# Optimization experiments

Measured on AMD Instinct MI355X. Metric: run time of the kernel, lower is better.

## Reference

```python
import jax, jax.numpy as jnp
import numpy as np

WS = 8      # window size
SS = 4      # shift size
NH = 4      # num heads
EPS = 1e-5
MLP_RATIO = 4


def _win_part(x, ws):
    # x: [B,D,H,W,C] -> [B*nD*nH*nW, ws^3, C]
    B, D, H, W, C = x.shape
    x = x.reshape(B, D // ws, ws, H // ws, ws, W // ws, ws, C)
    x = x.transpose(0, 1, 3, 5, 2, 4, 6, 7)
    return x.reshape(-1, ws * ws * ws, C)


def _win_rev(w, ws, B, D, H, W):
    C = w.shape[-1]
    x = w.reshape(B, D // ws, H // ws, W // ws, ws, ws, ws, C)
    x = x.transpose(0, 1, 4, 2, 5, 3, 6, 7)
    return x.reshape(B, D, H, W, C)


def _ln(x, g, b):
    m = jnp.mean(x, axis=-1, keepdims=True)
    v = jnp.mean((x - m) ** 2, axis=-1, keepdims=True)
    return (x - m) / jnp.sqrt(v + EPS) * g + b


def _rel_index(ws):
    coords = np.stack(np.meshgrid(np.arange(ws), np.arange(ws), np.arange(ws), indexing='ij'))  # [3,ws,ws,ws]
    cf = coords.reshape(3, -1)                      # [3, ws^3]
    rel = (cf[:, :, None] - cf[:, None, :]).transpose(1, 2, 0) + (ws - 1)  # [N,N,3]
    return rel[..., 0] * (2 * ws - 1) ** 2 + rel[..., 1] * (2 * ws - 1) + rel[..., 2]


def _attn_mask(D, H, W, ws, ss):
    img = np.zeros((1, D, H, W, 1), dtype=np.float32)
    cnt = 0
    sl = (slice(0, -ws), slice(-ws, -ss), slice(-ss, None))
    for d in sl:
        for h in sl:
            for w in sl:
                img[:, d, h, w, :] = cnt
                cnt += 1
    mw = np.asarray(_win_part(jnp.asarray(img), ws))[..., 0]  # [nW, ws^3]
    diff = mw[:, None, :] - mw[:, :, None]
    return np.where(diff != 0, -100.0, 0.0).astype(np.float32)


def setup_inputs() -> dict:
    key = jax.random.key(0)
    ks = jax.random.split(key, 12)
    B, D, H, W, C = 1, 16, 64, 64, 128
    mh = MLP_RATIO * C
    s = 0.02
    return {
        'x': jax.random.normal(ks[0], (B, D, H, W, C), jnp.float32),
        'attn_mask': jnp.asarray(_attn_mask(D, H, W, WS, SS)),
        'rel_index': jnp.asarray(_rel_index(WS), jnp.int32),
        'rel_bias': jax.random.normal(ks[1], ((2 * WS - 1) ** 3, NH), jnp.float32) * s,
        'qkv_w': jax.random.normal(ks[2], (3 * C, C), jnp.float32) * s,
        'qkv_b': jnp.zeros((3 * C,), jnp.float32),
        'proj_w': jax.random.normal(ks[3], (C, C), jnp.float32) * s,
        'proj_b': jnp.zeros((C,), jnp.float32),
        'norm1_g': jnp.ones((C,), jnp.float32),
        'norm1_b': jnp.zeros((C,), jnp.float32),
        'norm2_g': jnp.ones((C,), jnp.float32),
        'norm2_b': jnp.zeros((C,), jnp.float32),
        'mlp_w1': jax.random.normal(ks[4], (mh, C), jnp.float32) * s,
        'mlp_b1': jnp.zeros((mh,), jnp.float32),
        'mlp_w2': jax.random.normal(ks[5], (C, mh), jnp.float32) * s,
        'mlp_b2': jnp.zeros((C,), jnp.float32),
    }


def reference(x, attn_mask, rel_index, rel_bias, qkv_w, qkv_b, proj_w, proj_b,
              norm1_g, norm1_b, norm2_g, norm2_b, mlp_w1, mlp_b1, mlp_w2, mlp_b2):
    B, D, H, W, C = x.shape
    ws, ss, nh = WS, SS, NH
    hd = C // nh
    scale = hd ** -0.5
    N = ws ** 3
    shortcut = x
    h = _ln(x, norm1_g, norm1_b)
    h = jnp.roll(h, (-ss, -ss, -ss), axis=(1, 2, 3))
    xw = _win_part(h, ws)                 # [B_, N, C]
    B_ = xw.shape[0]
    nW = attn_mask.shape[0]
    qkv = xw @ qkv_w.T + qkv_b            # [B_, N, 3C]
    qkv = qkv.reshape(B_, N, 3, nh, hd).transpose(2, 0, 3, 1, 4)  # [3,B_,h,N,hd]
    q, k, v = qkv[0] * scale, qkv[1], qkv[2]
    attn = jnp.einsum('bhnd,bhmd->bhnm', q, k)
    rpe = rel_bias[rel_index.reshape(-1)].reshape(N, N, nh).transpose(2, 0, 1)  # [h,N,N]
    attn = attn + rpe[None]
    attn = attn.reshape(B_ // nW, nW, nh, N, N) + attn_mask[None, :, None]
    attn = jax.nn.softmax(attn.reshape(B_, nh, N, N), axis=-1)
    out = jnp.einsum('bhnm,bhmd->bhnd', attn, v).transpose(0, 2, 1, 3).reshape(B_, N, C)
    out = out @ proj_w.T + proj_b
    out = _win_rev(out, ws, B, D, H, W)
    out = jnp.roll(out, (ss, ss, ss), axis=(1, 2, 3))
    x = shortcut + out
    h2 = _ln(x, norm2_g, norm2_b)
    h2 = jax.nn.gelu(h2 @ mlp_w1.T + mlp_b1, approximate=False)
    return x + h2 @ mlp_w2.T + mlp_b2
```

## Files before the change

### kernel.cpp

```cpp
#include <hip/hip_runtime.h>
#include <math.h>

typedef __bf16 bf16;
typedef __bf16 bf16x4 __attribute__((ext_vector_type(4)));
typedef __bf16 bf16x8 __attribute__((ext_vector_type(8)));
typedef float f32x4 __attribute__((ext_vector_type(4)));
typedef unsigned short u16;
typedef u16 u16x2 __attribute__((ext_vector_type(2)));

#define LOG2E 1.4426950408889634f

__device__ __forceinline__ float b2f(u16 b) {
  return (float)__builtin_bit_cast(bf16, b);
}

__global__ void sniff_k(const unsigned* __restrict__ xw_, int* __restrict__ flag) {
  int lane = threadIdx.x;
  int c = 0;
#pragma unroll
  for (int j = 0; j < 4; j++) {
    unsigned e = (xw_[lane * 4 + j] >> 7) & 0xFFu;
    c += (e >= 100u && e <= 140u) ? 1 : 0;
  }
#pragma unroll
  for (int d = 1; d < 64; d <<= 1) c += __shfl_xor(c, d);
  if (lane == 0) *flag = (c >= 150) ? 1 : 0;
}

__global__ __launch_bounds__(256) void canon_norm_k(
    const void* __restrict__ sg, const void* __restrict__ sb,
    bf16* __restrict__ dg, bf16* __restrict__ db, const int* __restrict__ flag) {
  int i = threadIdx.x;
  int fl = *flag;
  if (i < 128) {
    dg[i] = fl ? ((const bf16*)sg)[i] : (bf16)((const float*)sg)[i];
  } else {
    int j = i - 128;
    db[j] = fl ? ((const bf16*)sb)[j] : (bf16)((const float*)sb)[j];
  }
}

struct ProArgs {
  const int* ridx;
  const void* rbias;
  bf16* rpem;
  const void* x;
  const bf16* g1;
  const bf16* b1n;
  bf16* xw;
  const void* csrc[12];
  bf16* cdst[12];
  int cn[12];
};

__global__ __launch_bounds__(256) void pro_k(ProArgs a,
                                             const int* __restrict__ flag) {
  const int bx = blockIdx.x, tid = threadIdx.x;
  const int fl = *flag;
  if (bx < 8192) {
    int t = bx * 256 + tid;
    int m0 = (t & 127) * 4, q = (t >> 7) & 511, h = (t >> 16) & 3, ty = t >> 18;
    int qd = q >> 6, qh = (q >> 3) & 7, qw = q & 7;
    int kt = m0 >> 6, mt = (m0 >> 4) & 3, quad = (m0 >> 2) & 3;
    int4 ri = *(const int4*)&a.ridx[q * 512 + m0];
    const int rv[4] = {ri.x, ri.y, ri.z, ri.w};
    bf16x4 o;
#pragma unroll
    for (int j = 0; j < 4; j++) {
      int m = m0 + j;
      int md = m >> 6, mh = (m >> 3) & 7, mw = m & 7;
      bool diff = ((ty & 4) && ((qd < 4) != (md < 4))) ||
                  ((ty & 2) && ((qh < 4) != (mh < 4))) ||
                  ((ty & 1) && ((qw < 4) != (mw < 4)));
      float bv = fl ? (float)((const bf16*)a.rbias)[rv[j] * 4 + h]
                    : ((const float*)a.rbias)[rv[j] * 4 + h];
      float v = bv * LOG2E;
      o[j] = (bf16)(v + (diff ? -144.2695041f : 0.f));
    }
    size_t out = ((size_t)(ty * 4 + h) << 18) +
                 (((size_t)(kt * 4 + quad) * 512 + q) * 16 + mt * 4);
    *(bf16x4*)&a.rpem[out] = o;
  } else if (bx < 24576) {
    int wave = tid >> 6, lane = tid & 63;
    int tok = (bx - 8192) * 4 + wave;
    int win = tok >> 9, pos = tok & 511;
    int rd = (win >> 6) * 8 + (pos >> 6);
    int rh = ((win >> 3) & 7) * 8 + ((pos >> 3) & 7);
    int rw = (win & 7) * 8 + (pos & 7);
    int od = (rd + 4) & 15, oh = (rh + 4) & 63, ow = (rw + 4) & 63;
    size_t src = (size_t)((od * 64 + oh) * 64 + ow) * 128;
    int ch = lane * 2;
    float f0, f1;
    if (!fl) {
      const float* xf = (const float*)a.x + src + ch;
      f0 = xf[0];
      f1 = xf[1];
    } else {
      u16x2 xv = *(const u16x2*)((const bf16*)a.x + src + ch);
      f0 = b2f(xv[0]);
      f1 = b2f(xv[1]);
    }
    float s = f0 + f1, sq = f0 * f0 + f1 * f1;
#pragma unroll
    for (int d = 1; d < 64; d <<= 1) {
      s += __shfl_xor(s, d);
      sq += __shfl_xor(sq, d);
    }
    float mean = s * (1.f / 128.f);
    float var = sq * (1.f / 128.f) - mean * mean;
    float rstd = rsqrtf(fmaxf(var, 0.f) + 1e-5f);
    u16x2 gv = *(const u16x2*)(a.g1 + ch), bv = *(const u16x2*)(a.b1n + ch);
    u16x2 ov;
    ov[0] =
        __builtin_bit_cast(u16, (bf16)((f0 - mean) * rstd * b2f(gv[0]) + b2f(bv[0])));
    ov[1] =
        __builtin_bit_cast(u16, (bf16)((f1 - mean) * rstd * b2f(gv[1]) + b2f(bv[1])));
    *(u16x2*)(a.xw + (size_t)tok * 128 + ch) = ov;
  } else {
    int seg = bx - 24576;
    int ti = seg >> 8;
    int i = (seg & 255) * 256 + tid;
    if (i < a.cn[ti]) {
      if (fl)
        a.cdst[ti][i] = ((const bf16*)a.csrc[ti])[i];
      else
        a.cdst[ti][i] = (bf16)((const float*)a.csrc[ti])[i];
    }
  }
}

template <int EPI, int BM, int BK, int N_, int K_>
__global__ __launch_bounds__(256) void gemm_k(const bf16* __restrict__ A,
                                              const bf16* __restrict__ B,
                                              const bf16* __restrict__ bias,
                                              void* __restrict__ outv,
                                              const void* __restrict__ residv,
                                              const int* __restrict__ flag) {
  constexpr int NC = K_ / BK;
  constexpr int NBUF = (NC > 1) ? 2 : 1;
  __shared__ __align__(16) u16 SM[NBUF][(BM + 128) * BK];
  const int t = threadIdx.x;
  const int wave = t >> 6, lane = t & 63, l15 = lane & 15, quad = lane >> 4;
  const int m0 = blockIdx.x * BM, n0 = blockIdx.y * 128;
  constexpr int MI = BM / 32;
  int fl = 0;
  if constexpr (EPI == 1) fl = *flag;
  f32x4 acc[MI][4] = {};
  const int wr = (wave >> 1) * (BM / 2), wc = (wave & 1) * 64;
  constexpr int TPR = BK / 8;
  constexpr int RPP = 256 / TPR;
  constexpr int PASSES = (BM + 128) / RPP;
  const int srow = t / TPR, sc16 = t % TPR;

  auto stage = [&](int c, int buf) {
#pragma unroll
    for (int p = 0; p < PASSES; p++) {
      int row = p * RPP + srow;
      int cs = sc16 ^ (row & 7);
      const u16* src;
      if (row < BM)
        src = (const u16*)A + (size_t)(m0 + row) * K_ + c * BK + cs * 8;
      else
        src = (const u16*)B + (size_t)(n0 + row - BM) * K_ + c * BK + cs * 8;
      __builtin_amdgcn_global_load_lds(
          (const __attribute__((address_space(1))) void*)src,
          (__attribute__((address_space(3))) void*)&SM[buf][row * BK + sc16 * 8],
          16, 0, 0);
    }
  };

  stage(0, 0);
  __syncthreads();
#pragma unroll
  for (int c = 0; c < NC; c++) {
    if (c + 1 < NC) stage(c + 1, (c + 1) & 1);
    const char* cur = (const char*)SM[c & 1];
#pragma unroll
    for (int ks = 0; ks < BK / 32; ks++) {
      bf16x8 a[MI], b[4];
#pragma unroll
      for (int i = 0; i < MI; i++) {
        int row = wr + i * 16 + l15;
        a[i] = *(const bf16x8*)(cur + row * (BK * 2) +
                                (((ks * 4 + quad) ^ (row & 7)) << 4));
      }
#pragma unroll
      for (int j = 0; j < 4; j++) {
        int row = BM + wc + j * 16 + l15;
        b[j] = *(const bf16x8*)(cur + row * (BK * 2) +
                                (((ks * 4 + quad) ^ (row & 7)) << 4));
      }
#pragma unroll
      for (int i = 0; i < MI; i++)
#pragma unroll
        for (int j = 0; j < 4; j++)
          acc[i][j] =
              __builtin_amdgcn_mfma_f32_16x16x32_bf16(a[i], b[j], acc[i][j], 0, 0, 0);
    }
    if (c + 1 < NC) __syncthreads();
  }
  const float qscale = 0.17677669529663687f * LOG2E;
#pragma unroll
  for (int i = 0; i < MI; i++) {
#pragma unroll
    for (int r = 0; r < 4; r++) {
      int tok = m0 + wr + i * 16 + quad * 4 + r;
      size_t obase = 0;
      if constexpr (EPI == 1) {
        int win = tok >> 9, pos = tok & 511;
        int rd = (win >> 6) * 8 + (pos >> 6);
        int rh = ((win >> 3) & 7) * 8 + ((pos >> 3) & 7);
        int rw = (win & 7) * 8 + (pos & 7);
        int od = (rd + 4) & 15, oh = (rh + 4) & 63, ow = (rw + 4) & 63;
        obase = (size_t)((od * 64 + oh) * 64 + ow) * 128;
      }
#pragma unroll
      for (int j = 0; j < 4; j++) {
        int gn = n0 + wc + j * 16 + l15;
        float v = acc[i][j][r] + (float)bias[gn];
        if constexpr (EPI == 0) {
          int tensor = gn >> 7, c = gn & 127, head = c >> 5, d = c & 31;
          if (tensor == 0) v *= qscale;
          int win = tok >> 9, pos = tok & 511;
          size_t off = ((((size_t)tensor * 4 + head) * 128 + win) * 512 + pos) * 32 + d;
          ((bf16*)outv)[off] = (bf16)v;
        } else {
          float rs = fl ? (float)((const bf16*)residv)[obase + gn]
                        : ((const float*)residv)[obase + gn];
          v += rs;
          ((bf16*)outv)[obase + gn] = (bf16)v;
        }
      }
    }
  }
}

__global__ __launch_bounds__(256) void mlp_k(const bf16* __restrict__ X2,
                                             const bf16* __restrict__ G2,
                                             const bf16* __restrict__ B2n,
                                             const bf16* __restrict__ W1,
                                             const bf16* __restrict__ B1,
                                             const bf16* __restrict__ W2,
                                             const bf16* __restrict__ B2,
                                             void* __restrict__ outv,
                                             const int* __restrict__ flag) {
  __shared__ __align__(16) u16 sA[32 * 128];
  __shared__ __align__(16) u16 sB[128 * 128];
  __shared__ __align__(16) u16 sH[32 * 520];
  const int t = threadIdx.x;
  const int wave = t >> 6, lane = t & 63, l15 = lane & 15, quad = lane >> 4;
  const int m0 = blockIdx.x * 32;
  const int wr = (wave >> 1) * 16, wc = (wave & 1) * 64;
  const int fl = *flag;
  const int srow = t >> 4, sc16 = t & 15;

  {
#pragma unroll
    for (int p = 0; p < 2; p++) {
      int row = p * 16 + srow;
      int cs = sc16 ^ (row & 7);
      __builtin_amdgcn_global_load_lds(
          (const __attribute__((address_space(1))) void*)((const u16*)X2 +
                                                          (size_t)(m0 + row) * 128 +
                                                          cs * 8),
          (__attribute__((address_space(3))) void*)&sA[row * 128 + sc16 * 8], 16,
          0, 0);
    }
#pragma unroll
    for (int p = 0; p < 8; p++) {
      int row = p * 16 + srow;
      int cs = sc16 ^ (row & 7);
      __builtin_amdgcn_global_load_lds(
          (const __attribute__((address_space(1))) void*)((const u16*)W1 +
                                                          (size_t)row * 128 +
                                                          cs * 8),
          (__attribute__((address_space(3))) void*)&sB[row * 128 + sc16 * 8], 16,
          0, 0);
    }
  }
  __syncthreads();

  {
    int r = t >> 3, k = t & 7;
    bf16x8 c0 = *(const bf16x8*)&sA[r * 128 + (k * 2 + 0) * 8];
    bf16x8 c1 = *(const bf16x8*)&sA[r * 128 + (k * 2 + 1) * 8];
    float s = 0.f, sq = 0.f;
#pragma unroll
    for (int e = 0; e < 8; e++) {
      float f0 = (float)c0[e], f1 = (float)c1[e];
      s += f0 + f1;
      sq += f0 * f0 + f1 * f1;
    }
#pragma unroll
    for (int d = 1; d < 8; d <<= 1) {
      s += __shfl_xor(s, d);
      sq += __shfl_xor(sq, d);
    }
    float mean = s * (1.f / 128.f);
    float var = sq * (1.f / 128.f) - mean * mean;
    float rstd = rsqrtf(fmaxf(var, 0.f) + 1e-5f);
    __syncthreads();
#pragma unroll
    for (int j = 0; j < 2; j++) {
      int tc = ((k * 2 + j) ^ (r & 7)) * 8;
      bf16x8 gv = *(const bf16x8*)&G2[tc];
      bf16x8 bv = *(const bf16x8*)&B2n[tc];
      bf16x8 cv = j ? c1 : c0;
      bf16x8 ov;
#pragma unroll
      for (int e = 0; e < 8; e++)
        ov[e] = (bf16)(((float)cv[e] - mean) * rstd * (float)gv[e] + (float)bv[e]);
      *(bf16x8*)&sA[r * 128 + (k * 2 + j) * 8] = ov;
    }
  }
  __syncthreads();

  bf16x8 wreg[8];

#pragma unroll 1
  for (int nc = 0; nc < 4; nc++) {
    {
      const bf16* Wn = (nc < 3) ? W1 : W2;
      const int chunk = (nc < 3) ? nc + 1 : 0;
      const int wK = (nc < 3) ? 128 : 512;
#pragma unroll
      for (int p = 0; p < 8; p++) {
        int row = p * 16 + srow;
        int cs = sc16 ^ (row & 7);
        const u16* src = (const u16*)Wn +
                         (size_t)(wK == 128 ? (chunk * 128 + row) : row) * wK +
                         (wK == 128 ? 0 : chunk * 128) + cs * 8;
        wreg[p] = *(const bf16x8*)src;
      }
    }
    f32x4 acc1[4] = {};
#pragma unroll
    for (int ks = 0; ks < 4; ks++) {
      int arow = wr + l15;
      bf16x8 av = *(const bf16x8*)((const char*)sA + arow * 256 +
                                   (((ks * 4 + quad) ^ (arow & 7)) << 4));
      bf16x8 bv[4];
#pragma unroll
      for (int j = 0; j < 4; j++) {
        int row = wc + j * 16 + l15;
        bv[j] = *(const bf16x8*)((const char*)sB + row * 256 +
                                 (((ks * 4 + quad) ^ (row & 7)) << 4));
      }
#pragma unroll
      for (int j = 0; j < 4; j++)
        acc1[j] = __builtin_amdgcn_mfma_f32_16x16x32_bf16(av, bv[j], acc1[j], 0, 0, 0);
    }
#pragma unroll
    for (int j = 0; j < 4; j++) {
      int ncol = nc * 128 + wc + j * 16 + l15;
      float bj = (float)B1[ncol];
#pragma unroll
      for (int r = 0; r < 4; r++) {
        float v = acc1[j][r] + bj;
        float v2 = v * v;
        float u2 = v * (2.30220806f + 0.10294323f * v2);
        float e2 = exp2f(u2);
        v = v - v * __builtin_amdgcn_rcpf(e2 + 1.f);
        sH[(wr + quad * 4 + r) * 520 + ncol] = __builtin_bit_cast(u16, (bf16)v);
      }
    }
    __syncthreads();
#pragma unroll
    for (int p = 0; p < 8; p++) {
      int row = p * 16 + srow;
      *(bf16x8*)&sB[row * 128 + sc16 * 8] = wreg[p];
    }
    __syncthreads();
  }

  f32x4 acc2[4] = {};
#pragma unroll 1
  for (int kc = 0; kc < 4; kc++) {
    if (kc < 3) {
      const int chunk = kc + 1;
#pragma unroll
      for (int p = 0; p < 8; p++) {
        int row = p * 16 + srow;
        int cs = sc16 ^ (row & 7);
        const u16* src =
            (const u16*)W2 + (size_t)row * 512 + chunk * 128 + cs * 8;
        wreg[p] = *(const bf16x8*)src;
      }
    }
#pragma unroll
    for (int ks = 0; ks < 4; ks++) {
      int arow = wr + l15;
      bf16x8 av = *(const bf16x8*)((const char*)sH + arow * 1040 +
                                   (kc * 128 + ks * 32 + quad * 8) * 2);
#pragma unroll
      for (int j = 0; j < 4; j++) {
        int row = wc + j * 16 + l15;
        bf16x8 bv = *(const bf16x8*)((const char*)sB + row * 256 +
                                     (((ks * 4 + quad) ^ (row & 7)) << 4));
        acc2[j] = __builtin_amdgcn_mfma_f32_16x16x32_bf16(av, bv, acc2[j], 0, 0, 0);
      }
    }
    if (kc < 3) {
      __syncthreads();
#pragma unroll
      for (int p = 0; p < 8; p++) {
        int row = p * 16 + srow;
        *(bf16x8*)&sB[row * 128 + sc16 * 8] = wreg[p];
      }
      __syncthreads();
    }
  }
#pragma unroll
  for (int j = 0; j < 4; j++) {
    int gn = wc + j * 16 + l15;
    float bj = (float)B2[gn];
#pragma unroll
    for (int r = 0; r < 4; r++) {
      int tok = m0 + wr + quad * 4 + r;
      size_t off = (size_t)tok * 128 + gn;
      float v = acc2[j][r] + bj + (float)X2[off];
      if (fl)
        ((bf16*)outv)[off] = (bf16)v;
      else
        ((float*)outv)[off] = v;
    }
  }
}

__global__ __launch_bounds__(512, 4) void attn_k(const bf16* __restrict__ qkv,
                                                 const bf16* __restrict__ rpem,
                                                 bf16* __restrict__ att) {
  __shared__ __align__(16) bf16 sVt[32 * 512];
  __shared__ __align__(16) bf16 sP[8][32 * 64];
  const int t = threadIdx.x;
  const int p = blockIdx.x;
  const int win = ((p >> 5) << 3) | (p & 7);
  const int head = (p >> 3) & 3;
  const int wave = t >> 6, lane = t & 63, l15 = lane & 15, quad = lane >> 4;

  const int wd = win >> 6, wh = (win >> 3) & 7, ww = win & 7;
  const int type = ((wd == 1) << 2) | ((wh == 7) << 1) | (ww == 7);

  const size_t hw32 = (size_t)512 * 32;
  const bf16* qp = qkv + ((size_t)(0 * 4 + head) * 128 + win) * hw32;
  const bf16* kp = qkv + ((size_t)(1 * 4 + head) * 128 + win) * hw32;
  const bf16* vp = qkv + ((size_t)(2 * 4 + head) * 128 + win) * hw32;
  const bf16* rpeh = rpem + ((size_t)(type * 4 + head) << 18);

  {
    int kpi = t >> 3, dblk = (t & 7) * 4;
    char* sb = (char*)sVt;
#pragma unroll
    for (int kb = 0; kb < 4; kb++) {
      const bf16* v0 = vp + (size_t)(kb * 128 + 2 * kpi) * 32 + dblk;
      bf16x4 a = *(const bf16x4*)v0;
      bf16x4 b = *(const bf16x4*)(v0 + 32);
      int keyw = kb * 64 + kpi;
#pragma unroll
      for (int dd = 0; dd < 4; dd++) {
        int row = dblk + dd;
        unsigned wv = (unsigned)__builtin_bit_cast(u16, a[dd]) |
                      ((unsigned)__builtin_bit_cast(u16, b[dd]) << 16);
        *(unsigned*)(sb + ((row * 1024 + keyw * 4) ^ ((row & 7) << 4))) = wv;
      }
    }
  }

  bf16x8 ones;
#pragma unroll
  for (int e = 0; e < 8; e++) ones[e] = (bf16)1.0f;

  __syncthreads();

  char* pw = (char*)sP[wave];
  const char* sv = (const char*)sVt;
  const int swz = (l15 & 7) << 4;

#pragma unroll 1
  for (int qh = 0; qh < 2; qh++) {
    const int qbase = qh * 256 + wave * 32;
    bf16x8 qa[2];
#pragma unroll
    for (int nt = 0; nt < 2; nt++)
      qa[nt] =
          *(const bf16x8*)(qp + (size_t)(qbase + nt * 16 + l15) * 32 + quad * 8);

    f32x4 O[2][2] = {};
    f32x4 O2[2] = {};

#pragma unroll 1
    for (int kt = 0; kt < 8; kt++) {
      bf16x8 kb[4];
      bf16x8 rv8[2][2];
#pragma unroll
      for (int mt = 0; mt < 4; mt++)
        kb[mt] = *(const bf16x8*)(kp + (size_t)(kt * 64 + mt * 16 + l15) * 32 +
                                  quad * 8);
#pragma unroll
      for (int nt = 0; nt < 2; nt++) {
        const bf16* rb =
            rpeh + ((size_t)(kt * 4 + quad) * 512 + (qbase + nt * 16 + l15)) * 16;
        rv8[nt][0] = *(const bf16x8*)rb;
        rv8[nt][1] = *(const bf16x8*)(rb + 8);
      }
      f32x4 S[4][2];
#pragma unroll
      for (int mt = 0; mt < 4; mt++)
#pragma unroll
        for (int nt = 0; nt < 2; nt++) {
          f32x4 c;
#pragma unroll
          for (int r = 0; r < 4; r++)
            c[r] = (float)rv8[nt][mt >> 1][(mt & 1) * 4 + r];
          S[mt][nt] =
              __builtin_amdgcn_mfma_f32_16x16x32_bf16(kb[mt], qa[nt], c, 0, 0, 0);
        }
#pragma unroll
      for (int nt = 0; nt < 2; nt++)
#pragma unroll
        for (int mt = 0; mt < 4; mt++) {
          bf16x4 pv;
#pragma unroll
          for (int r = 0; r < 4; r++) pv[r] = (bf16)exp2f(S[mt][nt][r]);
          *(bf16x4*)(pw + (((nt * 16 + l15) * 128 + mt * 32 + quad * 8) ^ swz)) =
              pv;
        }
#pragma unroll
      for (int s = 0; s < 2; s++) {
        int vc = kt * 128 + s * 64 + quad * 16;
        int pc = s * 64 + quad * 16;
        bf16x8 va0 = *(const bf16x8*)(sv + ((l15 * 1024 + vc) ^ swz));
        bf16x8 va1 = *(const bf16x8*)(sv + (((16 + l15) * 1024 + vc) ^ swz));
        bf16x8 pb0 = *(const bf16x8*)(pw + ((l15 * 128 + pc) ^ swz));
        bf16x8 pb1 = *(const bf16x8*)(pw + (((16 + l15) * 128 + pc) ^ swz));
        O[0][0] = __builtin_amdgcn_mfma_f32_16x16x32_bf16(va0, pb0, O[0][0], 0, 0, 0);
        O[0][1] = __builtin_amdgcn_mfma_f32_16x16x32_bf16(va0, pb1, O[0][1], 0, 0, 0);
        O[1][0] = __builtin_amdgcn_mfma_f32_16x16x32_bf16(va1, pb0, O[1][0], 0, 0, 0);
        O[1][1] = __builtin_amdgcn_mfma_f32_16x16x32_bf16(va1, pb1, O[1][1], 0, 0, 0);
        O2[0] = __builtin_amdgcn_mfma_f32_16x16x32_bf16(ones, pb0, O2[0], 0, 0, 0);
        O2[1] = __builtin_amdgcn_mfma_f32_16x16x32_bf16(ones, pb1, O2[1], 0, 0, 0);
      }
    }
#pragma unroll
    for (int nt = 0; nt < 2; nt++) {
      float inv = __builtin_amdgcn_rcpf(O2[nt][0]);
      int q = qbase + nt * 16 + l15;
#pragma unroll
      for (int dm = 0; dm < 2; dm++) {
        bf16x4 o;
#pragma unroll
        for (int r = 0; r < 4; r++) o[r] = (bf16)(O[dm][nt][r] * inv);
        *(bf16x4*)(att + ((size_t)win * 512 + q) * 128 + head * 32 + dm * 16 +
                   quad * 4) = o;
      }
    }
  }
}

extern "C" void kernel_launch(void* const* d_in, const int* in_sizes, int n_in,
                              void* d_out, int out_size, void* d_ws,
                              size_t ws_size, hipStream_t stream) {
  const int* rel_index = (const int*)d_in[2];
  char* w = (char*)d_ws;

  int* flag = (int*)w;
  bf16* qw_c = (bf16*)(w + (128ull << 10));
  bf16* pw_c = (bf16*)(w + (256ull << 10));
  bf16* w1_c = (bf16*)(w + (320ull << 10));
  bf16* w2_c = (bf16*)(w + (512ull << 10));
  bf16* qb_c = (bf16*)(w + (704ull << 10));
  bf16* pb_c = (bf16*)(w + (708ull << 10));
  bf16* g1_c = (bf16*)(w + (712ull << 10));
  bf16* b1n_c = (bf16*)(w + (716ull << 10));
  bf16* g2_c = (bf16*)(w + (720ull << 10));
  bf16* b2n_c = (bf16*)(w + (724ull << 10));
  bf16* mb1_c = (bf16*)(w + (728ull << 10));
  bf16* mb2_c = (bf16*)(w + (732ull << 10));
  bf16* xw = (bf16*)(w + (17ull << 20));
  bf16* qkvb = (bf16*)(w + (33ull << 20));
  bf16* x2 = (bf16*)(w + (99ull << 20));
  bf16* rpem = x2;
  bf16* att = xw;

  sniff_k<<<1, 64, 0, stream>>>((const unsigned*)d_in[0], flag);
  canon_norm_k<<<1, 256, 0, stream>>>(d_in[8], d_in[9], g1_c, b1n_c, flag);

  ProArgs pa;
  pa.ridx = rel_index;
  pa.rbias = d_in[3];
  pa.rpem = rpem;
  pa.x = d_in[0];
  pa.g1 = g1_c;
  pa.b1n = b1n_c;
  pa.xw = xw;
  const int srcidx[12] = {4, 5, 6, 7, 8, 9, 10, 11, 12, 13, 14, 15};
  bf16* dsts[12] = {qw_c, qb_c, pw_c, pb_c, g1_c, b1n_c,
                    g2_c, b2n_c, w1_c, mb1_c, w2_c, mb2_c};
  for (int i = 0; i < 12; i++) {
    pa.csrc[i] = d_in[srcidx[i]];
    pa.cdst[i] = dsts[i];
    pa.cn[i] = in_sizes[srcidx[i]];
  }
  pro_k<<<27648, 256, 0, stream>>>(pa, flag);

  gemm_k<0, 32, 128, 384, 128><<<dim3(2048, 3), 256, 0, stream>>>(
      xw, qw_c, qb_c, qkvb, nullptr, flag);
  attn_k<<<512, 512, 0, stream>>>(qkvb, rpem, att);
  gemm_k<1, 32, 128, 128, 128><<<dim3(2048, 1), 256, 0, stream>>>(
      att, pw_c, pb_c, x2, d_in[0], flag);
  mlp_k<<<2048, 256, 0, stream>>>(x2, g2_c, b2n_c, w1_c, mb1_c, w2_c, mb2_c,
                                  d_out, flag);
}
```

Before: 376.3 us.

## Fuse LayerNorm1, shift and window gather into the QKV GEMM prologue

```diff
diff --git a/kernel.cpp b/kernel.cpp
--- a/kernel.cpp
+++ b/kernel.cpp
@@ -27,27 +27,10 @@
   if (lane == 0) *flag = (c >= 150) ? 1 : 0;
 }
 
-__global__ __launch_bounds__(256) void canon_norm_k(
-    const void* __restrict__ sg, const void* __restrict__ sb,
-    bf16* __restrict__ dg, bf16* __restrict__ db, const int* __restrict__ flag) {
-  int i = threadIdx.x;
-  int fl = *flag;
-  if (i < 128) {
-    dg[i] = fl ? ((const bf16*)sg)[i] : (bf16)((const float*)sg)[i];
-  } else {
-    int j = i - 128;
-    db[j] = fl ? ((const bf16*)sb)[j] : (bf16)((const float*)sb)[j];
-  }
-}
-
 struct ProArgs {
   const int* ridx;
   const void* rbias;
   bf16* rpem;
-  const void* x;
-  const bf16* g1;
-  const bf16* b1n;
-  bf16* xw;
   const void* csrc[12];
   bf16* cdst[12];
   int cn[12];
@@ -80,44 +63,8 @@
     size_t out = ((size_t)(ty * 4 + h) << 18) +
                  (((size_t)(kt * 4 + quad) * 512 + q) * 16 + mt * 4);
     *(bf16x4*)&a.rpem[out] = o;
-  } else if (bx < 24576) {
-    int wave = tid >> 6, lane = tid & 63;
-    int tok = (bx - 8192) * 4 + wave;
-    int win = tok >> 9, pos = tok & 511;
-    int rd = (win >> 6) * 8 + (pos >> 6);
-    int rh = ((win >> 3) & 7) * 8 + ((pos >> 3) & 7);
-    int rw = (win & 7) * 8 + (pos & 7);
-    int od = (rd + 4) & 15, oh = (rh + 4) & 63, ow = (rw + 4) & 63;
-    size_t src = (size_t)((od * 64 + oh) * 64 + ow) * 128;
-    int ch = lane * 2;
-    float f0, f1;
-    if (!fl) {
-      const float* xf = (const float*)a.x + src + ch;
-      f0 = xf[0];
-      f1 = xf[1];
-    } else {
-      u16x2 xv = *(const u16x2*)((const bf16*)a.x + src + ch);
-      f0 = b2f(xv[0]);
-      f1 = b2f(xv[1]);
-    }
-    float s = f0 + f1, sq = f0 * f0 + f1 * f1;
-#pragma unroll
-    for (int d = 1; d < 64; d <<= 1) {
-      s += __shfl_xor(s, d);
-      sq += __shfl_xor(sq, d);
-    }
-    float mean = s * (1.f / 128.f);
-    float var = sq * (1.f / 128.f) - mean * mean;
-    float rstd = rsqrtf(fmaxf(var, 0.f) + 1e-5f);
-    u16x2 gv = *(const u16x2*)(a.g1 + ch), bv = *(const u16x2*)(a.b1n + ch);
-    u16x2 ov;
-    ov[0] =
-        __builtin_bit_cast(u16, (bf16)((f0 - mean) * rstd * b2f(gv[0]) + b2f(bv[0])));
-    ov[1] =
-        __builtin_bit_cast(u16, (bf16)((f1 - mean) * rstd * b2f(gv[1]) + b2f(bv[1])));
-    *(u16x2*)(a.xw + (size_t)tok * 128 + ch) = ov;
   } else {
-    int seg = bx - 24576;
+    int seg = bx - 8192;
     int ti = seg >> 8;
     int i = (seg & 255) * 256 + tid;
     if (i < a.cn[ti]) {
@@ -129,108 +76,186 @@
   }
 }
 
-template <int EPI, int BM, int BK, int N_, int K_>
-__global__ __launch_bounds__(256) void gemm_k(const bf16* __restrict__ A,
+__global__ __launch_bounds__(256) void qkv_k(const void* __restrict__ X,
+                                             const bf16* __restrict__ G1,
+                                             const bf16* __restrict__ B1n,
+                                             const bf16* __restrict__ B,
+                                             const bf16* __restrict__ bias,
+                                             bf16* __restrict__ outv,
+                                             const int* __restrict__ flag) {
+  __shared__ __align__(16) u16 SM[160 * 128];
+  const int t = threadIdx.x;
+  const int wave = t >> 6, lane = t & 63, l15 = lane & 15, quad = lane >> 4;
+  const int m0 = blockIdx.x * 32, n0 = blockIdx.y * 128;
+  const int fl = *flag;
+  f32x4 acc[4] = {};
+  const int wr = (wave >> 1) * 16, wc = (wave & 1) * 64;
+  const int srow = t >> 4, sc16 = t & 15;
+
+#pragma unroll
+  for (int p = 0; p < 8; p++) {
+    int row = 32 + p * 16 + srow;
+    int cs = sc16 ^ (row & 7);
+    __builtin_amdgcn_global_load_lds(
+        (const __attribute__((address_space(1))) void*)((const u16*)B +
+                                                        (size_t)(n0 + row - 32) *
+                                                            128 +
+                                                        cs * 8),
+        (__attribute__((address_space(3))) void*)&SM[row * 128 + sc16 * 8], 16,
+        0, 0);
+  }
+
+  {
+    int row = t >> 3, k = t & 7;
+    int tok = m0 + row;
+    int win = tok >> 9, pos = tok & 511;
+    int rd = (win >> 6) * 8 + (pos >> 6);
+    int rh = ((win >> 3) & 7) * 8 + ((pos >> 3) & 7);
+    int rw = (win & 7) * 8 + (pos & 7);
+    int od = (rd + 4) & 15, oh = (rh + 4) & 63, ow = (rw + 4) & 63;
+    size_t src = (size_t)((od * 64 + oh) * 64 + ow) * 128;
+    float f[16];
+    if (fl) {
+      bf16x8 v0 = *(const bf16x8*)((const bf16*)X + src + (k * 2 + 0) * 8);
+      bf16x8 v1 = *(const bf16x8*)((const bf16*)X + src + (k * 2 + 1) * 8);
+#pragma unroll
+      for (int e = 0; e < 8; e++) {
+        f[e] = (float)v0[e];
+        f[8 + e] = (float)v1[e];
+      }
+    } else {
+      const float* xf = (const float*)X + src + k * 16;
+      f32x4 a0 = *(const f32x4*)(xf + 0), a1 = *(const f32x4*)(xf + 4);
+      f32x4 a2 = *(const f32x4*)(xf + 8), a3 = *(const f32x4*)(xf + 12);
+#pragma unroll
+      for (int e = 0; e < 4; e++) {
+        f[e] = a0[e];
+        f[4 + e] = a1[e];
+        f[8 + e] = a2[e];
+        f[12 + e] = a3[e];
+      }
+    }
+    float s = 0.f, sq = 0.f;
+#pragma unroll
+    for (int e = 0; e < 16; e++) {
+      s += f[e];
+      sq += f[e] * f[e];
+    }
+#pragma unroll
+    for (int d = 1; d < 8; d <<= 1) {
+      s += __shfl_xor(s, d);
+      sq += __shfl_xor(sq, d);
+    }
+    float mean = s * (1.f / 128.f);
+    float var = sq * (1.f / 128.f) - mean * mean;
+    float rstd = rsqrtf(fmaxf(var, 0.f) + 1e-5f);
+#pragma unroll
+    for (int j = 0; j < 2; j++) {
+      int c = k * 2 + j;
+      bf16x8 gv = *(const bf16x8*)&G1[c * 8];
+      bf16x8 bv = *(const bf16x8*)&B1n[c * 8];
+      bf16x8 ov;
+#pragma unroll
+      for (int e = 0; e < 8; e++)
+        ov[e] = (bf16)((f[j * 8 + e] - mean) * rstd * (float)gv[e] + (float)bv[e]);
+      *(bf16x8*)&SM[row * 128 + (c ^ (row & 7)) * 8] = ov;
+    }
+  }
+  __syncthreads();
+
+  const char* cur = (const char*)SM;
+#pragma unroll
+  for (int ks = 0; ks < 4; ks++) {
+    int arow = wr + l15;
+    bf16x8 a = *(const bf16x8*)(cur + arow * 256 +
+                                (((ks * 4 + quad) ^ (arow & 7)) << 4));
+#pragma unroll
+    for (int j = 0; j < 4; j++) {
+      int row = 32 + wc + j * 16 + l15;
+      bf16x8 b = *(const bf16x8*)(cur + row * 256 +
+                                  (((ks * 4 + quad) ^ (row & 7)) << 4));
+      acc[j] = __builtin_amdgcn_mfma_f32_16x16x32_bf16(a, b, acc[j], 0, 0, 0);
+    }
+  }
+  const float qscale = 0.17677669529663687f * LOG2E;
+#pragma unroll
+  for (int r = 0; r < 4; r++) {
+    int tok = m0 + wr + quad * 4 + r;
+    int win = tok >> 9, pos = tok & 511;
+#pragma unroll
+    for (int j = 0; j < 4; j++) {
+      int gn = n0 + wc + j * 16 + l15;
+      float v = acc[j][r] + (float)bias[gn];
+      int tensor = gn >> 7, c = gn & 127, head = c >> 5, d = c & 31;
+      if (tensor == 0) v *= qscale;
+      size_t off = ((((size_t)tensor * 4 + head) * 128 + win) * 512 + pos) * 32 + d;
+      outv[off] = (bf16)v;
+    }
+  }
+}
+
+__global__ __launch_bounds__(256) void proj_k(const bf16* __restrict__ A,
                                               const bf16* __restrict__ B,
                                               const bf16* __restrict__ bias,
-                                              void* __restrict__ outv,
+                                              bf16* __restrict__ outv,
                                               const void* __restrict__ residv,
                                               const int* __restrict__ flag) {
-  constexpr int NC = K_ / BK;
-  constexpr int NBUF = (NC > 1) ? 2 : 1;
-  __shared__ __align__(16) u16 SM[NBUF][(BM + 128) * BK];
+  __shared__ __align__(16) u16 SM[160 * 128];
   const int t = threadIdx.x;
   const int wave = t >> 6, lane = t & 63, l15 = lane & 15, quad = lane >> 4;
-  const int m0 = blockIdx.x * BM, n0 = blockIdx.y * 128;
-  constexpr int MI = BM / 32;
-  int fl = 0;
-  if constexpr (EPI == 1) fl = *flag;
-  f32x4 acc[MI][4] = {};
-  const int wr = (wave >> 1) * (BM / 2), wc = (wave & 1) * 64;
-  constexpr int TPR = BK / 8;
-  constexpr int RPP = 256 / TPR;
-  constexpr int PASSES = (BM + 128) / RPP;
-  const int srow = t / TPR, sc16 = t % TPR;
-
-  auto stage = [&](int c, int buf) {
-#pragma unroll
-    for (int p = 0; p < PASSES; p++) {
-      int row = p * RPP + srow;
-      int cs = sc16 ^ (row & 7);
-      const u16* src;
-      if (row < BM)
-        src = (const u16*)A + (size_t)(m0 + row) * K_ + c * BK + cs * 8;
-      else
-        src = (const u16*)B + (size_t)(n0 + row - BM) * K_ + c * BK + cs * 8;
-      __builtin_amdgcn_global_load_lds(
-          (const __attribute__((address_space(1))) void*)src,
-          (__attribute__((address_space(3))) void*)&SM[buf][row * BK + sc16 * 8],
-          16, 0, 0);
-    }
-  };
-
-  stage(0, 0);
+  const int m0 = blockIdx.x * 32, n0 = 0;
+  const int fl = *flag;
+  f32x4 acc[4] = {};
+  const int wr = (wave >> 1) * 16, wc = (wave & 1) * 64;
+  const int srow = t >> 4, sc16 = t & 15;
+
+#pragma unroll
+  for (int p = 0; p < 10; p++) {
+    int row = p * 16 + srow;
+    int cs = sc16 ^ (row & 7);
+    const u16* src;
+    if (row < 32)
+      src = (const u16*)A + (size_t)(m0 + row) * 128 + cs * 8;
+    else
+      src = (const u16*)B + (size_t)(n0 + row - 32) * 128 + cs * 8;
+    __builtin_amdgcn_global_load_lds(
+        (const __attribute__((address_space(1))) void*)src,
+        (__attribute__((address_space(3))) void*)&SM[row * 128 + sc16 * 8], 16,
+        0, 0);
+  }
   __syncthreads();
-#pragma unroll
-  for (int c = 0; c < NC; c++) {
-    if (c + 1 < NC) stage(c + 1, (c + 1) & 1);
-    const char* cur = (const char*)SM[c & 1];
-#pragma unroll
-    for (int ks = 0; ks < BK / 32; ks++) {
-      bf16x8 a[MI], b[4];
-#pragma unroll
-      for (int i = 0; i < MI; i++) {
-        int row = wr + i * 16 + l15;
-        a[i] = *(const bf16x8*)(cur + row * (BK * 2) +
-                                (((ks * 4 + quad) ^ (row & 7)) << 4));
-      }
-#pragma unroll
-      for (int j = 0; j < 4; j++) {
-        int row = BM + wc + j * 16 + l15;
-        b[j] = *(const bf16x8*)(cur + row * (BK * 2) +
-                                (((ks * 4 + quad) ^ (row & 7)) << 4));
-      }
-#pragma unroll
-      for (int i = 0; i < MI; i++)
-#pragma unroll
-        for (int j = 0; j < 4; j++)
-          acc[i][j] =
-              __builtin_amdgcn_mfma_f32_16x16x32_bf16(a[i], b[j], acc[i][j], 0, 0, 0);
-    }
-    if (c + 1 < NC) __syncthreads();
-  }
-  const float qscale = 0.17677669529663687f * LOG2E;
-#pragma unroll
-  for (int i = 0; i < MI; i++) {
-#pragma unroll
-    for (int r = 0; r < 4; r++) {
-      int tok = m0 + wr + i * 16 + quad * 4 + r;
-      size_t obase = 0;
-      if constexpr (EPI == 1) {
-        int win = tok >> 9, pos = tok & 511;
-        int rd = (win >> 6) * 8 + (pos >> 6);
-        int rh = ((win >> 3) & 7) * 8 + ((pos >> 3) & 7);
-        int rw = (win & 7) * 8 + (pos & 7);
-        int od = (rd + 4) & 15, oh = (rh + 4) & 63, ow = (rw + 4) & 63;
-        obase = (size_t)((od * 64 + oh) * 64 + ow) * 128;
-      }
-#pragma unroll
-      for (int j = 0; j < 4; j++) {
-        int gn = n0 + wc + j * 16 + l15;
-        float v = acc[i][j][r] + (float)bias[gn];
-        if constexpr (EPI == 0) {
-          int tensor = gn >> 7, c = gn & 127, head = c >> 5, d = c & 31;
-          if (tensor == 0) v *= qscale;
-          int win = tok >> 9, pos = tok & 511;
-          size_t off = ((((size_t)tensor * 4 + head) * 128 + win) * 512 + pos) * 32 + d;
-          ((bf16*)outv)[off] = (bf16)v;
-        } else {
-          float rs = fl ? (float)((const bf16*)residv)[obase + gn]
-                        : ((const float*)residv)[obase + gn];
-          v += rs;
-          ((bf16*)outv)[obase + gn] = (bf16)v;
-        }
-      }
+
+  const char* cur = (const char*)SM;
+#pragma unroll
+  for (int ks = 0; ks < 4; ks++) {
+    int arow = wr + l15;
+    bf16x8 a = *(const bf16x8*)(cur + arow * 256 +
+                                (((ks * 4 + quad) ^ (arow & 7)) << 4));
+#pragma unroll
+    for (int j = 0; j < 4; j++) {
+      int row = 32 + wc + j * 16 + l15;
+      bf16x8 b = *(const bf16x8*)(cur + row * 256 +
+                                  (((ks * 4 + quad) ^ (row & 7)) << 4));
+      acc[j] = __builtin_amdgcn_mfma_f32_16x16x32_bf16(a, b, acc[j], 0, 0, 0);
+    }
+  }
+#pragma unroll
+  for (int r = 0; r < 4; r++) {
+    int tok = m0 + wr + quad * 4 + r;
+    int win = tok >> 9, pos = tok & 511;
+    int rd = (win >> 6) * 8 + (pos >> 6);
+    int rh = ((win >> 3) & 7) * 8 + ((pos >> 3) & 7);
+    int rw = (win & 7) * 8 + (pos & 7);
+    int od = (rd + 4) & 15, oh = (rh + 4) & 63, ow = (rw + 4) & 63;
+    size_t obase = (size_t)((od * 64 + oh) * 64 + ow) * 128;
+#pragma unroll
+    for (int j = 0; j < 4; j++) {
+      int gn = wc + j * 16 + l15;
+      float v = acc[j][r] + (float)bias[gn];
+      float rs = fl ? (float)((const bf16*)residv)[obase + gn]
+                    : ((const float*)residv)[obase + gn];
+      v += rs;
+      outv[obase + gn] = (bf16)v;
     }
   }
 }
@@ -583,16 +608,11 @@
   bf16* att = xw;
 
   sniff_k<<<1, 64, 0, stream>>>((const unsigned*)d_in[0], flag);
-  canon_norm_k<<<1, 256, 0, stream>>>(d_in[8], d_in[9], g1_c, b1n_c, flag);
 
   ProArgs pa;
   pa.ridx = rel_index;
   pa.rbias = d_in[3];
   pa.rpem = rpem;
-  pa.x = d_in[0];
-  pa.g1 = g1_c;
-  pa.b1n = b1n_c;
-  pa.xw = xw;
   const int srcidx[12] = {4, 5, 6, 7, 8, 9, 10, 11, 12, 13, 14, 15};
   bf16* dsts[12] = {qw_c, qb_c, pw_c, pb_c, g1_c, b1n_c,
                     g2_c, b2n_c, w1_c, mb1_c, w2_c, mb2_c};
@@ -601,13 +621,12 @@
     pa.cdst[i] = dsts[i];
     pa.cn[i] = in_sizes[srcidx[i]];
   }
-  pro_k<<<27648, 256, 0, stream>>>(pa, flag);
-
-  gemm_k<0, 32, 128, 384, 128><<<dim3(2048, 3), 256, 0, stream>>>(
-      xw, qw_c, qb_c, qkvb, nullptr, flag);
+  pro_k<<<11264, 256, 0, stream>>>(pa, flag);
+
+  qkv_k<<<dim3(2048, 3), 256, 0, stream>>>(d_in[0], g1_c, b1n_c, qw_c, qb_c,
+                                           qkvb, flag);
   attn_k<<<512, 512, 0, stream>>>(qkvb, rpem, att);
-  gemm_k<1, 32, 128, 128, 128><<<dim3(2048, 1), 256, 0, stream>>>(
-      att, pw_c, pb_c, x2, d_in[0], flag);
+  proj_k<<<2048, 256, 0, stream>>>(att, pw_c, pb_c, x2, d_in[0], flag);
   mlp_k<<<2048, 256, 0, stream>>>(x2, g2_c, b2n_c, w1_c, mb1_c, w2_c, mb2_c,
                                   d_out, flag);
 }
```

Result: no change. 374.2 us (-0.6%).
